# Kernel optimization log

Hardware: AMD Instinct MI355X
Metric: run time of the kernel (lower is better)

Reference implementation:

```python
import jax, jax.numpy as jnp
import numpy as np

N = 100000      # n_nodes
E = 1600000     # n_edges (avg degree 16)
D_IN, D_H, D_OUT = 128, 64, 16


def setup_inputs() -> dict:
    key = jax.random.key(0)
    k1, k2, k3, k4 = jax.random.split(key, 4)
    x = jax.random.normal(k1, (N, D_IN), dtype=jnp.float32)
    edge_index = jax.random.randint(k2, (2, E), 0, N, dtype=jnp.int32)
    W1 = jax.random.normal(k3, (D_IN, D_H), dtype=jnp.float32) / np.sqrt(D_IN)
    b1 = jnp.zeros((D_H,), dtype=jnp.float32)
    W2 = jax.random.normal(k4, (D_H, D_OUT), dtype=jnp.float32) / np.sqrt(D_H)
    b2 = jnp.zeros((D_OUT,), dtype=jnp.float32)
    return {"x": x, "edge_index": edge_index, "W1": W1, "b1": b1, "W2": W2, "b2": b2}


def gcn_conv(x, src, dst, W, b, n):
    """PyG GCNConv: linear transform, then deg^-1/2 A deg^-1/2 aggregation, + bias.
    src/dst already include self-loops."""
    h = x @ W                                              # [n, d_out]
    deg = jax.ops.segment_sum(jnp.ones_like(dst, dtype=h.dtype), dst, num_segments=n)
    dinv = jnp.where(deg > 0, jax.lax.rsqrt(jnp.maximum(deg, 1.0)), 0.0)
    norm = dinv[src] * dinv[dst]                           # [E+n]
    msgs = h[src] * norm[:, None]                          # gather + scale
    out = jax.ops.segment_sum(msgs, dst, num_segments=n)   # scatter-add
    return out + b


def reference(x, edge_index, W1, b1, W2, b2):
    loops = jnp.arange(N, dtype=edge_index.dtype)
    src = jnp.concatenate([edge_index[0], loops])
    dst = jnp.concatenate([edge_index[1], loops])
    h = jax.nn.relu(gcn_conv(x, src, dst, W1, b1, N))
    return gcn_conv(h, src, dst, W2, b2, N)
```

## Files before the change

kernel.cpp:

```cpp
#include <hip/hip_runtime.h>
#include <cstdint>

#define N_NODES 100000
#define N_EDGES 1600000
#define D_IN    128
#define D_H     64
#define D_OUT   16
#define M_TILES 6250

#define NBKT   512
#define NPB    196
#define BCAP   4096
#define TILE_E 4096
#define NTILES ((N_EDGES + TILE_E - 1) / TILE_E)
#define G1     256

typedef __attribute__((ext_vector_type(8))) short short8;
typedef __attribute__((ext_vector_type(4))) float floatx4;

static __device__ __forceinline__ unsigned short f2bf(float f) {
    unsigned int u = __float_as_uint(f);
    u = u + 0x7FFFu + ((u >> 16) & 1u);
    return (unsigned short)(u >> 16);
}
static __device__ __forceinline__ float bf2f(unsigned short h) {
    return __uint_as_float(((unsigned int)h) << 16);
}


__global__ __launch_bounds__(512) void zero_small_kernel(int* __restrict__ cursors,
                                                         int* __restrict__ srcs) {
    cursors[threadIdx.x] = 0;
    if (threadIdx.x < 16) srcs[N_EDGES + threadIdx.x] = 0;
}

__global__ __launch_bounds__(256) void bin_kernel(const int* __restrict__ src,
                                                  const int* __restrict__ dst,
                                                  int* __restrict__ cursors,
                                                  int* __restrict__ region) {
    __shared__ int hcnt[NBKT];
    __shared__ int hbase[NBKT];
    const int t = threadIdx.x;
    for (int tile = blockIdx.x; tile < NTILES; tile += gridDim.x) {
        for (int i = t; i < NBKT; i += 256) hcnt[i] = 0;
        __syncthreads();
        int e0 = tile * TILE_E + t * 16;
        int pk[16], bk[16], rk[16];
        bool full = (e0 + 16 <= N_EDGES);
        if (full) {
            const int4* dp = (const int4*)(dst + e0);
            const int4* sp = (const int4*)(src + e0);
            int dv[16], sv[16];
            #pragma unroll
            for (int q = 0; q < 4; ++q) {
                int4 d4 = dp[q]; int4 s4 = sp[q];
                dv[4*q+0]=d4.x; dv[4*q+1]=d4.y; dv[4*q+2]=d4.z; dv[4*q+3]=d4.w;
                sv[4*q+0]=s4.x; sv[4*q+1]=s4.y; sv[4*q+2]=s4.z; sv[4*q+3]=s4.w;
            }
            #pragma unroll
            for (int k = 0; k < 16; ++k) {
                int d = dv[k];
                int b = d / NPB;
                bk[k] = b;
                pk[k] = ((d - b * NPB) << 17) | sv[k];
                rk[k] = atomicAdd(&hcnt[b], 1);
            }
        }
        __syncthreads();
        for (int i = t; i < NBKT; i += 256) {
            int c = hcnt[i];
            if (c > 0) hbase[i] = atomicAdd(&cursors[i], c);
        }
        __syncthreads();
        if (full) {
            #pragma unroll
            for (int k = 0; k < 16; ++k)
                region[bk[k] * BCAP + hbase[bk[k]] + rk[k]] = pk[k];
        }
        __syncthreads();
    }
}

__global__ __launch_bounds__(256) void build_kernel(const int* __restrict__ cursors,
                                                    const int* __restrict__ region,
                                                    int* __restrict__ offsets,
                                                    float* __restrict__ dinv,
                                                    int* __restrict__ srcs) {
    __shared__ int lhist[NPB];
    __shared__ int lscan[NPB + 1];
    __shared__ int sbuf[256];
    __shared__ int srt[BCAP];
    __shared__ int red[4];
    int b = blockIdx.x;
    int t = threadIdx.x;

    int c0 = cursors[t];
    int c1 = cursors[t + 256];
    int p = ((t < b) ? c0 : 0) + ((t + 256 < b) ? c1 : 0);
    int lane = t & 63, wid = t >> 6;
    #pragma unroll
    for (int off = 32; off > 0; off >>= 1) p += __shfl_down(p, off);
    if (lane == 0) red[wid] = p;
    __syncthreads();
    int base = red[0] + red[1] + red[2] + red[3];
    int cnt = cursors[b];
    const int* reg = region + b * BCAP;

    for (int i = t; i < NPB; i += 256) lhist[i] = 0;
    __syncthreads();
    for (int i = t; i < cnt; i += 256) {
        int ln = reg[i] >> 17;
        atomicAdd(&lhist[ln], 1);
    }
    __syncthreads();
    int v = (t < NPB) ? lhist[t] : 0;
    sbuf[t] = v;
    __syncthreads();
    for (int off = 1; off < 256; off <<= 1) {
        int u = (t >= off) ? sbuf[t - off] : 0;
        __syncthreads();
        sbuf[t] += u;
        __syncthreads();
    }
    int incl = sbuf[t];
    if (t < NPB) lscan[t] = incl - v;
    if (t == NPB - 1) lscan[NPB] = incl;
    __syncthreads();
    if (t < NPB) lhist[t] = incl - v;
    __syncthreads();

    int node0 = b * NPB;
    int nlim = N_NODES - node0;
    if (nlim > NPB) nlim = NPB;
    if (t < nlim) {
        offsets[node0 + t] = base + lscan[t];
        int c = lscan[t + 1] - lscan[t];
        dinv[node0 + t] = rsqrtf((float)c + 1.0f);
    }
    if (b == (N_NODES - 1) / NPB && t == 0) offsets[N_NODES] = base + cnt;

    for (int i = t; i < cnt; i += 256) {
        int pk = reg[i];
        int ln = pk >> 17;
        int pos = atomicAdd(&lhist[ln], 1);
        srt[pos] = pk & 0x1FFFF;
    }
    __syncthreads();
    for (int i = t; i < cnt; i += 256) srcs[base + i] = srt[i];
}

__global__ __launch_bounds__(256) void gemm1_mfma_kernel(const float* __restrict__ x,
                                                         const float* __restrict__ W1,
                                                         const float* __restrict__ dinv,
                                                         unsigned short* __restrict__ hs) {
    __shared__ unsigned short bhi_lds[8192];
    __shared__ unsigned short blo_lds[8192];

    for (int e = threadIdx.x; e < 8192; e += 256) {
        int j    = e & 7;
        int lane = (e >> 3) & 63;
        int pair = e >> 9;
        int kc   = pair >> 2;
        int nt   = pair & 3;
        int k = kc * 32 + (lane >> 4) * 8 + j;
        int n = nt * 16 + (lane & 15);
        float w = W1[k * D_H + n];
        unsigned short hi = f2bf(w);
        float lo = w - bf2f(hi);
        bhi_lds[e] = hi;
        blo_lds[e] = f2bf(lo);
    }
    __syncthreads();

    int wid  = threadIdx.x >> 6;
    int lane = threadIdx.x & 63;
    int quad = lane >> 4;
    int m    = lane & 15;

    int tile = blockIdx.x * 4 + wid;
    if (tile >= M_TILES) return;
    int mbase = tile * 16;

    const float* xr = x + (size_t)(mbase + m) * D_IN + quad * 8;
    short8 ahi[4], alo[4];
    #pragma unroll
    for (int kc = 0; kc < 4; ++kc) {
        floatx4 v0 = *(const floatx4*)(xr + kc * 32);
        floatx4 v1 = *(const floatx4*)(xr + kc * 32 + 4);
        float f[8] = {v0.x, v0.y, v0.z, v0.w, v1.x, v1.y, v1.z, v1.w};
        #pragma unroll
        for (int j = 0; j < 8; ++j) {
            unsigned short hi = f2bf(f[j]);
            float lo = f[j] - bf2f(hi);
            ahi[kc][j] = (short)hi;
            alo[kc][j] = (short)f2bf(lo);
        }
    }

    floatx4 acc[4] = {{0.f,0.f,0.f,0.f},{0.f,0.f,0.f,0.f},{0.f,0.f,0.f,0.f},{0.f,0.f,0.f,0.f}};
    #pragma unroll
    for (int kc = 0; kc < 4; ++kc) {
        #pragma unroll
        for (int nt = 0; nt < 4; ++nt) {
            int fo = ((kc * 4 + nt) * 64 + lane) * 8;
            short8 bhi = *(const short8*)&bhi_lds[fo];
            short8 blo = *(const short8*)&blo_lds[fo];
            acc[nt] = __builtin_amdgcn_mfma_f32_16x16x32_bf16(ahi[kc], bhi, acc[nt], 0, 0, 0);
            acc[nt] = __builtin_amdgcn_mfma_f32_16x16x32_bf16(ahi[kc], blo, acc[nt], 0, 0, 0);
            acc[nt] = __builtin_amdgcn_mfma_f32_16x16x32_bf16(alo[kc], bhi, acc[nt], 0, 0, 0);
        }
    }

    float dv[4];
    #pragma unroll
    for (int r = 0; r < 4; ++r) dv[r] = dinv[mbase + quad * 4 + r];
    #pragma unroll
    for (int nt = 0; nt < 4; ++nt) {
        int col = nt * 16 + m;
        #pragma unroll
        for (int r = 0; r < 4; ++r) {
            int row = mbase + quad * 4 + r;
            hs[row * D_H + col] = f2bf(acc[nt][r] * dv[r]);
        }
    }
}

__global__ __launch_bounds__(256) void agg1_fused_kernel(const unsigned short* __restrict__ hs,
                                                         const int* __restrict__ offsets,
                                                         const int* __restrict__ srcs,
                                                         const float* __restrict__ dinv,
                                                         const float* __restrict__ b1,
                                                         const float* __restrict__ W2,
                                                         float* __restrict__ h2s) {
    __shared__ float w2t[16 * 68];
    __shared__ float rbuf[16 * 68];

    const int tid = threadIdx.x;
    for (int i = tid; i < 1024; i += 256) {
        int j = i >> 4, c = i & 15;
        w2t[c * 68 + j] = W2[i];
    }

    const int g    = tid >> 4;
    const int sl   = tid & 15;
    const int node = blockIdx.x * 16 + g;
    const int c4   = sl * 4;

    const int beg = offsets[node];
    const int end = offsets[node + 1];

    ushort4 s4v = *(const ushort4*)(hs + (size_t)node * D_H + c4);
    float a0 = bf2f(s4v.x), a1 = bf2f(s4v.y), a2 = bf2f(s4v.z), a3 = bf2f(s4v.w);

    for (int e = beg; e < end; e += 16) {
        int rem = end - e;
        int idx = srcs[e + sl];
        #pragma unroll
        for (int k = 0; k < 16; ++k) {
            int j = __shfl(idx, k, 16);
            ushort4 v = *(const ushort4*)(hs + (size_t)j * D_H + c4);
            float m = (k < rem) ? 1.0f : 0.0f;
            a0 = fmaf(bf2f(v.x), m, a0);
            a1 = fmaf(bf2f(v.y), m, a1);
            a2 = fmaf(bf2f(v.z), m, a2);
            a3 = fmaf(bf2f(v.w), m, a3);
        }
    }

    const float dv = dinv[node];
    const floatx4 bb = *(const floatx4*)(b1 + c4);
    float* rb = rbuf + g * 68;
    rb[c4 + 0] = fmaxf(a0 * dv + bb.x, 0.f);
    rb[c4 + 1] = fmaxf(a1 * dv + bb.y, 0.f);
    rb[c4 + 2] = fmaxf(a2 * dv + bb.z, 0.f);
    rb[c4 + 3] = fmaxf(a3 * dv + bb.w, 0.f);
    __syncthreads();

    float p = 0.f;
    #pragma unroll
    for (int t4 = 0; t4 < 16; ++t4) {
        floatx4 rv = *(const floatx4*)(rb + 4 * t4);
        floatx4 wv = *(const floatx4*)(&w2t[sl * 68 + 4 * t4]);
        p += rv.x * wv.x + rv.y * wv.y + rv.z * wv.z + rv.w * wv.w;
    }
    h2s[node * D_OUT + sl] = p * dv;
}

__global__ __launch_bounds__(256) void agg2_kernel(const float* __restrict__ h2s,
                                                   const int* __restrict__ offsets,
                                                   const int* __restrict__ srcs,
                                                   const float* __restrict__ dinv,
                                                   const float* __restrict__ b2,
                                                   float* __restrict__ out) {
    int col = threadIdx.x & 15;
    int nidx = (blockIdx.x * blockDim.x + threadIdx.x) >> 4;
    int stride = (gridDim.x * blockDim.x) >> 4;
    for (int node = nidx; node < N_NODES; node += stride) {
        int beg = offsets[node], end = offsets[node + 1];
        float acc = h2s[node * D_OUT + col];
        for (int e = beg; e < end; e += 16) {
            int rem = end - e;
            const int* ep = srcs + e;
            int jj[16];
            #pragma unroll
            for (int k = 0; k < 16; ++k) jj[k] = ep[k];
            float vv[16];
            #pragma unroll
            for (int k = 0; k < 16; ++k) vv[k] = h2s[jj[k] * D_OUT + col];
            #pragma unroll
            for (int k = 0; k < 16; ++k) {
                float m = (k < rem) ? 1.0f : 0.0f;
                acc = fmaf(vv[k], m, acc);
            }
        }
        out[node * D_OUT + col] = acc * dinv[node] + b2[col];
    }
}

extern "C" void kernel_launch(void* const* d_in, const int* in_sizes, int n_in,
                              void* d_out, int out_size, void* d_ws, size_t ws_size,
                              hipStream_t stream) {
    const float* x  = (const float*)d_in[0];
    const int*   ei = (const int*)d_in[1];
    const float* W1 = (const float*)d_in[2];
    const float* b1 = (const float*)d_in[3];
    const float* W2 = (const float*)d_in[4];
    const float* b2 = (const float*)d_in[5];
    float* out = (float*)d_out;

    const int* src = ei;
    const int* dst = ei + N_EDGES;

    char* w = (char*)d_ws;
    int*   cursors  = (int*)(w + 0);
    int*   offsets  = (int*)(w + 4096);
    float* dinv     = (float*)(w + 404224);
    int*   srcs     = (int*)(w + 804224);
    unsigned short* hs = (unsigned short*)(w + 7204352);
    float* h2s      = (float*)(w + 20004480);
    int*   region   = (int*)(w + 26404480);

    zero_small_kernel<<<1, 512, 0, stream>>>(cursors, srcs);
    bin_kernel<<<G1, 256, 0, stream>>>(src, dst, cursors, region);
    build_kernel<<<NBKT, 256, 0, stream>>>(cursors, region, offsets, dinv, srcs);
    gemm1_mfma_kernel<<<(M_TILES + 3) / 4, 256, 0, stream>>>(x, W1, dinv, hs);
    agg1_fused_kernel<<<6250, 256, 0, stream>>>(hs, offsets, srcs, dinv, b1, W2, h2s);
    agg2_kernel<<<6250, 256, 0, stream>>>(h2s, offsets, srcs, dinv, b2, out);
}
```

Before: 200.9 us.

## Run GEMM1 concurrently with edge binning and defer source dinv scaling to aggregation

The binning pass and the first dense transform are merged into one launch. Blocks below G1 bin edges and the rest compute x@W1 with MFMA. Because dinv is not yet available at that point, GEMM1 now writes unscaled rows. The first aggregation then multiplies each neighbour by a gathered dinv[src] value broadcast with a shuffle. This lets the transform overlap the atomic-heavy binning and removes one launch, at the cost of an extra dinv gather per edge and more LDS per block for the fused kernel.

```diff
diff --git a/kernel.cpp b/kernel.cpp
--- a/kernel.cpp
+++ b/kernel.cpp
@@ -14,6 +14,7 @@
 #define TILE_E 4096
 #define NTILES ((N_EDGES + TILE_E - 1) / TILE_E)
 #define G1     256
+#define GEMM_BLOCKS ((M_TILES + 3) / 4)
 
 typedef __attribute__((ext_vector_type(8))) short short8;
 typedef __attribute__((ext_vector_type(4))) float floatx4;
@@ -34,50 +35,123 @@
     if (threadIdx.x < 16) srcs[N_EDGES + threadIdx.x] = 0;
 }
 
-__global__ __launch_bounds__(256) void bin_kernel(const int* __restrict__ src,
-                                                  const int* __restrict__ dst,
-                                                  int* __restrict__ cursors,
-                                                  int* __restrict__ region) {
+__global__ __launch_bounds__(256) void fused_bin_gemm1_kernel(
+        const int* __restrict__ src, const int* __restrict__ dst,
+        int* __restrict__ cursors, int* __restrict__ region,
+        const float* __restrict__ x, const float* __restrict__ W1,
+        unsigned short* __restrict__ hs) {
     __shared__ int hcnt[NBKT];
     __shared__ int hbase[NBKT];
+    __shared__ unsigned short bhi_lds[8192];
+    __shared__ unsigned short blo_lds[8192];
+
     const int t = threadIdx.x;
-    for (int tile = blockIdx.x; tile < NTILES; tile += gridDim.x) {
-        for (int i = t; i < NBKT; i += 256) hcnt[i] = 0;
-        __syncthreads();
-        int e0 = tile * TILE_E + t * 16;
-        int pk[16], bk[16], rk[16];
-        bool full = (e0 + 16 <= N_EDGES);
-        if (full) {
-            const int4* dp = (const int4*)(dst + e0);
-            const int4* sp = (const int4*)(src + e0);
-            int dv[16], sv[16];
-            #pragma unroll
-            for (int q = 0; q < 4; ++q) {
-                int4 d4 = dp[q]; int4 s4 = sp[q];
-                dv[4*q+0]=d4.x; dv[4*q+1]=d4.y; dv[4*q+2]=d4.z; dv[4*q+3]=d4.w;
-                sv[4*q+0]=s4.x; sv[4*q+1]=s4.y; sv[4*q+2]=s4.z; sv[4*q+3]=s4.w;
+
+    if (blockIdx.x < G1) {
+        for (int tile = blockIdx.x; tile < NTILES; tile += G1) {
+            for (int i = t; i < NBKT; i += 256) hcnt[i] = 0;
+            __syncthreads();
+            int e0 = tile * TILE_E + t * 16;
+            int pk[16], bk[16], rk[16];
+            bool full = (e0 + 16 <= N_EDGES);
+            if (full) {
+                const int4* dp = (const int4*)(dst + e0);
+                const int4* sp = (const int4*)(src + e0);
+                int dv[16], sv[16];
+                #pragma unroll
+                for (int q = 0; q < 4; ++q) {
+                    int4 d4 = dp[q]; int4 s4 = sp[q];
+                    dv[4*q+0]=d4.x; dv[4*q+1]=d4.y; dv[4*q+2]=d4.z; dv[4*q+3]=d4.w;
+                    sv[4*q+0]=s4.x; sv[4*q+1]=s4.y; sv[4*q+2]=s4.z; sv[4*q+3]=s4.w;
+                }
+                #pragma unroll
+                for (int k = 0; k < 16; ++k) {
+                    int d = dv[k];
+                    int b = d / NPB;
+                    bk[k] = b;
+                    pk[k] = ((d - b * NPB) << 17) | sv[k];
+                    rk[k] = atomicAdd(&hcnt[b], 1);
+                }
             }
-            #pragma unroll
-            for (int k = 0; k < 16; ++k) {
-                int d = dv[k];
-                int b = d / NPB;
-                bk[k] = b;
-                pk[k] = ((d - b * NPB) << 17) | sv[k];
-                rk[k] = atomicAdd(&hcnt[b], 1);
+            __syncthreads();
+            for (int i = t; i < NBKT; i += 256) {
+                int c = hcnt[i];
+                if (c > 0) hbase[i] = atomicAdd(&cursors[i], c);
             }
-        }
-        __syncthreads();
-        for (int i = t; i < NBKT; i += 256) {
-            int c = hcnt[i];
-            if (c > 0) hbase[i] = atomicAdd(&cursors[i], c);
-        }
-        __syncthreads();
-        if (full) {
-            #pragma unroll
-            for (int k = 0; k < 16; ++k)
-                region[bk[k] * BCAP + hbase[bk[k]] + rk[k]] = pk[k];
-        }
-        __syncthreads();
+            __syncthreads();
+            if (full) {
+                #pragma unroll
+                for (int k = 0; k < 16; ++k)
+                    region[bk[k] * BCAP + hbase[bk[k]] + rk[k]] = pk[k];
+            }
+            __syncthreads();
+        }
+        return;
+    }
+
+    for (int e = t; e < 8192; e += 256) {
+        int j    = e & 7;
+        int lane = (e >> 3) & 63;
+        int pair = e >> 9;
+        int kc   = pair >> 2;
+        int nt   = pair & 3;
+        int k = kc * 32 + (lane >> 4) * 8 + j;
+        int n = nt * 16 + (lane & 15);
+        float w = W1[k * D_H + n];
+        unsigned short hi = f2bf(w);
+        float lo = w - bf2f(hi);
+        bhi_lds[e] = hi;
+        blo_lds[e] = f2bf(lo);
+    }
+    __syncthreads();
+
+    int wid  = t >> 6;
+    int lane = t & 63;
+    int quad = lane >> 4;
+    int m    = lane & 15;
+
+    int tile = (blockIdx.x - G1) * 4 + wid;
+    if (tile >= M_TILES) return;
+    int mbase = tile * 16;
+
+    const float* xr = x + (size_t)(mbase + m) * D_IN + quad * 8;
+    short8 ahi[4], alo[4];
+    #pragma unroll
+    for (int kc = 0; kc < 4; ++kc) {
+        floatx4 v0 = *(const floatx4*)(xr + kc * 32);
+        floatx4 v1 = *(const floatx4*)(xr + kc * 32 + 4);
+        float f[8] = {v0.x, v0.y, v0.z, v0.w, v1.x, v1.y, v1.z, v1.w};
+        #pragma unroll
+        for (int j = 0; j < 8; ++j) {
+            unsigned short hi = f2bf(f[j]);
+            float lo = f[j] - bf2f(hi);
+            ahi[kc][j] = (short)hi;
+            alo[kc][j] = (short)f2bf(lo);
+        }
+    }
+
+    floatx4 acc[4] = {{0.f,0.f,0.f,0.f},{0.f,0.f,0.f,0.f},{0.f,0.f,0.f,0.f},{0.f,0.f,0.f,0.f}};
+    #pragma unroll
+    for (int kc = 0; kc < 4; ++kc) {
+        #pragma unroll
+        for (int nt = 0; nt < 4; ++nt) {
+            int fo = ((kc * 4 + nt) * 64 + lane) * 8;
+            short8 bhi = *(const short8*)&bhi_lds[fo];
+            short8 blo = *(const short8*)&blo_lds[fo];
+            acc[nt] = __builtin_amdgcn_mfma_f32_16x16x32_bf16(ahi[kc], bhi, acc[nt], 0, 0, 0);
+            acc[nt] = __builtin_amdgcn_mfma_f32_16x16x32_bf16(ahi[kc], blo, acc[nt], 0, 0, 0);
+            acc[nt] = __builtin_amdgcn_mfma_f32_16x16x32_bf16(alo[kc], bhi, acc[nt], 0, 0, 0);
+        }
+    }
+
+    #pragma unroll
+    for (int nt = 0; nt < 4; ++nt) {
+        int col = nt * 16 + m;
+        #pragma unroll
+        for (int r = 0; r < 4; ++r) {
+            int row = mbase + quad * 4 + r;
+            hs[row * D_H + col] = f2bf(acc[nt][r]);
+        }
     }
 }
 
@@ -149,82 +223,6 @@
     for (int i = t; i < cnt; i += 256) srcs[base + i] = srt[i];
 }
 
-__global__ __launch_bounds__(256) void gemm1_mfma_kernel(const float* __restrict__ x,
-                                                         const float* __restrict__ W1,
-                                                         const float* __restrict__ dinv,
-                                                         unsigned short* __restrict__ hs) {
-    __shared__ unsigned short bhi_lds[8192];
-    __shared__ unsigned short blo_lds[8192];
-
-    for (int e = threadIdx.x; e < 8192; e += 256) {
-        int j    = e & 7;
-        int lane = (e >> 3) & 63;
-        int pair = e >> 9;
-        int kc   = pair >> 2;
-        int nt   = pair & 3;
-        int k = kc * 32 + (lane >> 4) * 8 + j;
-        int n = nt * 16 + (lane & 15);
-        float w = W1[k * D_H + n];
-        unsigned short hi = f2bf(w);
-        float lo = w - bf2f(hi);
-        bhi_lds[e] = hi;
-        blo_lds[e] = f2bf(lo);
-    }
-    __syncthreads();
-
-    int wid  = threadIdx.x >> 6;
-    int lane = threadIdx.x & 63;
-    int quad = lane >> 4;
-    int m    = lane & 15;
-
-    int tile = blockIdx.x * 4 + wid;
-    if (tile >= M_TILES) return;
-    int mbase = tile * 16;
-
-    const float* xr = x + (size_t)(mbase + m) * D_IN + quad * 8;
-    short8 ahi[4], alo[4];
-    #pragma unroll
-    for (int kc = 0; kc < 4; ++kc) {
-        floatx4 v0 = *(const floatx4*)(xr + kc * 32);
-        floatx4 v1 = *(const floatx4*)(xr + kc * 32 + 4);
-        float f[8] = {v0.x, v0.y, v0.z, v0.w, v1.x, v1.y, v1.z, v1.w};
-        #pragma unroll
-        for (int j = 0; j < 8; ++j) {
-            unsigned short hi = f2bf(f[j]);
-            float lo = f[j] - bf2f(hi);
-            ahi[kc][j] = (short)hi;
-            alo[kc][j] = (short)f2bf(lo);
-        }
-    }
-
-    floatx4 acc[4] = {{0.f,0.f,0.f,0.f},{0.f,0.f,0.f,0.f},{0.f,0.f,0.f,0.f},{0.f,0.f,0.f,0.f}};
-    #pragma unroll
-    for (int kc = 0; kc < 4; ++kc) {
-        #pragma unroll
-        for (int nt = 0; nt < 4; ++nt) {
-            int fo = ((kc * 4 + nt) * 64 + lane) * 8;
-            short8 bhi = *(const short8*)&bhi_lds[fo];
-            short8 blo = *(const short8*)&blo_lds[fo];
-            acc[nt] = __builtin_amdgcn_mfma_f32_16x16x32_bf16(ahi[kc], bhi, acc[nt], 0, 0, 0);
-            acc[nt] = __builtin_amdgcn_mfma_f32_16x16x32_bf16(ahi[kc], blo, acc[nt], 0, 0, 0);
-            acc[nt] = __builtin_amdgcn_mfma_f32_16x16x32_bf16(alo[kc], bhi, acc[nt], 0, 0, 0);
-        }
-    }
-
-    float dv[4];
-    #pragma unroll
-    for (int r = 0; r < 4; ++r) dv[r] = dinv[mbase + quad * 4 + r];
-    #pragma unroll
-    for (int nt = 0; nt < 4; ++nt) {
-        int col = nt * 16 + m;
-        #pragma unroll
-        for (int r = 0; r < 4; ++r) {
-            int row = mbase + quad * 4 + r;
-            hs[row * D_H + col] = f2bf(acc[nt][r] * dv[r]);
-        }
-    }
-}
-
 __global__ __launch_bounds__(256) void agg1_fused_kernel(const unsigned short* __restrict__ hs,
                                                          const int* __restrict__ offsets,
                                                          const int* __restrict__ srcs,
@@ -248,18 +246,22 @@
 
     const int beg = offsets[node];
     const int end = offsets[node + 1];
+    const float dv = dinv[node];
 
     ushort4 s4v = *(const ushort4*)(hs + (size_t)node * D_H + c4);
-    float a0 = bf2f(s4v.x), a1 = bf2f(s4v.y), a2 = bf2f(s4v.z), a3 = bf2f(s4v.w);
+    float a0 = bf2f(s4v.x) * dv, a1 = bf2f(s4v.y) * dv;
+    float a2 = bf2f(s4v.z) * dv, a3 = bf2f(s4v.w) * dv;
 
     for (int e = beg; e < end; e += 16) {
         int rem = end - e;
         int idx = srcs[e + sl];
+        float dvv = dinv[idx];
         #pragma unroll
         for (int k = 0; k < 16; ++k) {
-            int j = __shfl(idx, k, 16);
+            int j   = __shfl(idx, k, 16);
+            float dj = __shfl(dvv, k, 16);
             ushort4 v = *(const ushort4*)(hs + (size_t)j * D_H + c4);
-            float m = (k < rem) ? 1.0f : 0.0f;
+            float m = (k < rem) ? dj : 0.0f;
             a0 = fmaf(bf2f(v.x), m, a0);
             a1 = fmaf(bf2f(v.y), m, a1);
             a2 = fmaf(bf2f(v.z), m, a2);
@@ -267,7 +269,6 @@
         }
     }
 
-    const float dv = dinv[node];
     const floatx4 bb = *(const floatx4*)(b1 + c4);
     float* rb = rbuf + g * 68;
     rb[c4 + 0] = fmaxf(a0 * dv + bb.x, 0.f);
@@ -341,9 +342,9 @@
     int*   region   = (int*)(w + 26404480);
 
     zero_small_kernel<<<1, 512, 0, stream>>>(cursors, srcs);
-    bin_kernel<<<G1, 256, 0, stream>>>(src, dst, cursors, region);
+    fused_bin_gemm1_kernel<<<G1 + GEMM_BLOCKS, 256, 0, stream>>>(
+        src, dst, cursors, region, x, W1, hs);
     build_kernel<<<NBKT, 256, 0, stream>>>(cursors, region, offsets, dinv, srcs);
-    gemm1_mfma_kernel<<<(M_TILES + 3) / 4, 256, 0, stream>>>(x, W1, dinv, hs);
     agg1_fused_kernel<<<6250, 256, 0, stream>>>(hs, offsets, srcs, dinv, b1, W2, h2s);
     agg2_kernel<<<6250, 256, 0, stream>>>(h2s, offsets, srcs, dinv, b2, out);
 }
```

Result: slower. 209.8 us (+4.4%).
